# Kernel tuning notes

Measured on AMD Instinct MI355X. Metric: run time of the kernel, lower is better.

## Reference

```python
import jax, jax.numpy as jnp
import numpy as np

B, W, H = 128, 512, 512


def setup_inputs() -> dict:
    key = jax.random.key(0)
    ks = jax.random.split(key, 10)
    s = 1.0 / np.sqrt(H)
    return {
        "g": jax.random.normal(ks[0], (B, H), jnp.float32),
        "c_g": jax.random.normal(ks[1], (B, H), jnp.float32),
        "h": jax.random.normal(ks[2], (B, W, H), jnp.float32),
        "c": jax.random.normal(ks[3], (B, W, H), jnp.float32),
        "W_w": jax.random.normal(ks[4], (2 * H, H), jnp.float32) * s,
        "w_w": jax.random.normal(ks[5], (H, H), jnp.float32) * s,
        "U_w": jax.random.normal(ks[6], (2 * H, H), jnp.float32) * s,
        "U_b": jax.random.normal(ks[7], (2 * H,), jnp.float32) * s,
        "u_w": jax.random.normal(ks[8], (H, H), jnp.float32) * s,
        "u_b": jax.random.normal(ks[9], (H,), jnp.float32) * s,
    }


def reference(g, c_g, h, c, W_w, w_w, U_w, U_b, u_w, u_b):
    hid = w_w.shape[0]
    # attn_pooling: mean over word dim -> [B, H]
    h_avg = jnp.mean(h, axis=-2)
    # gates f, o: [B, H] each
    fo = jax.nn.sigmoid(g @ W_w.T + h_avg @ U_w.T + U_b)
    f, o = fo[..., :hid], fo[..., hid:]
    # per-word forget weights, softmax over word dim: [B, W, H]
    f_w = jax.nn.sigmoid((g @ w_w.T)[..., None, :] + h @ u_w.T + u_b)
    f_w = jax.nn.softmax(f_w, axis=-2)
    new_c = f * c_g + jnp.sum(c * f_w, axis=-2)
    new_g = o * jnp.tanh(new_c)
    return new_g, new_c
```

## Files before the change

kernel.cpp:

```cpp
#include <hip/hip_runtime.h>
#include <stdint.h>

#define BB 128
#define WW 512
#define HH 512
#define TILE 128
#define BK 64

typedef __attribute__((ext_vector_type(8))) short bf16x8;
typedef __attribute__((ext_vector_type(4))) float f32x4;

__device__ __forceinline__ float bf2f(unsigned short u) {
  union { unsigned int i; float f; } v;
  v.i = ((unsigned int)u) << 16;
  return v.f;
}
__device__ __forceinline__ unsigned int pack_bf2(float lo, float hi) {
  union { float f; unsigned int u; } a, b;
  a.f = lo; b.f = hi;
  return (a.u >> 16) | (b.u & 0xFFFF0000u);
}
__device__ __forceinline__ float dot4v(float4 u, float4 v) {
  return u.x * v.x + u.y * v.y + u.z * v.z + u.w * v.w;
}
__device__ __forceinline__ void gload_lds16(const void* src, void* lds_dst) {
  __builtin_amdgcn_global_load_lds(
      (const __attribute__((address_space(1))) unsigned int*)src,
      (__attribute__((address_space(3))) unsigned int*)lds_dst, 16, 0, 0);
}

__global__ __launch_bounds__(256) void k01(
    const float* __restrict__ g, const float* __restrict__ W_w,
    const float* __restrict__ w_w, const float* __restrict__ u_w,
    float* __restrict__ gw, float* __restrict__ gfo,
    unsigned short* __restrict__ u_wb) {
  __shared__ __align__(16) unsigned short As[TILE * BK];
  __shared__ __align__(16) unsigned short Bs[TILE * BK];
  const int bid = blockIdx.x;
  const int t = threadIdx.x;

  if (bid >= 12) {
    const int cid0 = (bid - 12) * 256 + t;
    for (int idx = cid0; idx < 32768; idx += 16384) {
      const int tile = idx >> 11;
      const int rem  = idx & 2047;
      const int row  = rem >> 3;
      const int eg   = (rem & 7) * 8;
      const int nh   = tile >> 3;
      const int kt   = tile & 7;
      const int c0   = kt * 64 + (eg ^ ((row & 7) << 3));
      const float4* sp = (const float4*)(u_w + (size_t)(nh * 256 + row) * HH + c0);
      float4 s0 = sp[0], s1 = sp[1];
      uint4 pv;
      pv.x = pack_bf2(s0.x, s0.y); pv.y = pack_bf2(s0.z, s0.w);
      pv.z = pack_bf2(s1.x, s1.y); pv.w = pack_bf2(s1.z, s1.w);
      *(uint4*)(u_wb + (size_t)idx * 8) = pv;
    }
    return;
  }

  const int nc = bid;
  const int lane = t & 63, wave = t >> 6;
  const int wm = wave >> 1, wn = wave & 1;
  const int l15 = lane & 15, quad = lane >> 4;

  const float* wsrc = (nc < 4) ? (w_w + (size_t)nc * TILE * HH)
                               : (W_w + (size_t)(nc - 4) * TILE * HH);

  const f32x4 zero = {0.f, 0.f, 0.f, 0.f};
  f32x4 acc[4][4];
#pragma unroll
  for (int i = 0; i < 4; ++i)
#pragma unroll
    for (int j = 0; j < 4; ++j) acc[i][j] = zero;

  const int srow = t >> 3;
  const int scol = (t & 7) * 8;

  for (int kt = 0; kt < 8; ++kt) {
    const int k0 = kt * BK;
#pragma unroll
    for (int p = 0; p < 4; ++p) {
      const int row = p * 32 + srow;
      const float4* ap = (const float4*)(g    + (size_t)row * HH + k0 + scol);
      const float4* bp = (const float4*)(wsrc + (size_t)row * HH + k0 + scol);
      float4 a0 = ap[0], a1 = ap[1], b0 = bp[0], b1 = bp[1];
      uint4 av, bv;
      av.x = pack_bf2(a0.x, a0.y); av.y = pack_bf2(a0.z, a0.w);
      av.z = pack_bf2(a1.x, a1.y); av.w = pack_bf2(a1.z, a1.w);
      bv.x = pack_bf2(b0.x, b0.y); bv.y = pack_bf2(b0.z, b0.w);
      bv.z = pack_bf2(b1.x, b1.y); bv.w = pack_bf2(b1.z, b1.w);
      *(uint4*)(As + row * BK + scol) = av;
      *(uint4*)(Bs + row * BK + scol) = bv;
    }
    __syncthreads();
#pragma unroll
    for (int ks = 0; ks < 2; ++ks) {
      bf16x8 af[4], bg[4];
#pragma unroll
      for (int i = 0; i < 4; ++i)
        af[i] = *(const bf16x8*)(As + (wm * 64 + i * 16 + l15) * BK + ks * 32 + quad * 8);
#pragma unroll
      for (int j = 0; j < 4; ++j)
        bg[j] = *(const bf16x8*)(Bs + (wn * 64 + j * 16 + l15) * BK + ks * 32 + quad * 8);
#pragma unroll
      for (int i = 0; i < 4; ++i)
#pragma unroll
        for (int j = 0; j < 4; ++j)
          acc[i][j] = __builtin_amdgcn_mfma_f32_16x16x32_bf16(af[i], bg[j], acc[i][j], 0, 0, 0);
    }
    __syncthreads();
  }

#pragma unroll
  for (int j = 0; j < 4; ++j) {
    const int nl = wn * 64 + j * 16 + l15;
#pragma unroll
    for (int i = 0; i < 4; ++i) {
#pragma unroll
      for (int r = 0; r < 4; ++r) {
        const int b = wm * 64 + i * 16 + quad * 4 + r;
        const float v = acc[i][j][r];
        if (nc < 4) gw[(size_t)b * HH + nc * TILE + nl] = v;
        else        gfo[(size_t)b * 2 * HH + (nc - 4) * TILE + nl] = v;
      }
    }
  }
}

__global__ __launch_bounds__(512, 4) void k2_fused(
    const float* __restrict__ h, const float* __restrict__ c,
    const unsigned short* __restrict__ u_wb, const float* __restrict__ u_b,
    const float* __restrict__ gw,
    float* __restrict__ hsumP, float* __restrict__ denP, float* __restrict__ numP) {
  __shared__ __align__(16) unsigned short Bs[256 * 64];
  __shared__ __align__(16) unsigned short As[128 * 64];
  __shared__ float colred[8][64];
  __shared__ float redD[2][256];
  __shared__ float redN[2][256];

  const int bid = blockIdx.x;
  const int b  = bid >> 3;
  const int wc = (bid >> 1) & 3;
  const int nh = bid & 1;
  const int t = threadIdx.x;
  const int lane = t & 63, wave = t >> 6;
  const int wm = wave >> 2, wn = wave & 3;
  const int l15 = lane & 15, quad = lane >> 4;

  const size_t hbase = ((size_t)b * WW + (size_t)wc * 128) * HH;
  const unsigned short* ubase = u_wb + (size_t)nh * 8 * 16384;

  const f32x4 zero = {0.f, 0.f, 0.f, 0.f};
  f32x4 acc[4][4];
#pragma unroll
  for (int i = 0; i < 4; ++i)
#pragma unroll
    for (int j = 0; j < 4; ++j) acc[i][j] = zero;

  const int srow = t >> 3;
  const int scol = (t & 7) * 8;

  for (int kt = 0; kt < 8; ++kt) {
    const int k0 = kt * 64;

    if (nh == 0 && kt > 0 && t < 64) {
      float tot = 0.f;
#pragma unroll
      for (int gq = 0; gq < 8; ++gq) tot += colred[gq][t];
      hsumP[((size_t)b * 4 + wc) * HH + (kt - 1) * 64 + t] = tot;
    }

#pragma unroll
    for (int it = 0; it < 4; ++it) {
      const int s = wave * 4 + it;
      const unsigned short* src =
          ubase + ((size_t)kt * 16384 + (size_t)s * 512 + (size_t)lane * 8);
      gload_lds16(src, Bs + (size_t)s * 512);
    }

#pragma unroll
    for (int p = 0; p < 2; ++p) {
      const int row = p * 64 + srow;
      const float4* ap = (const float4*)(h + hbase + (size_t)row * HH + k0 + scol);
      float4 a0 = ap[0], a1 = ap[1];
      uint4 av;
      av.x = pack_bf2(a0.x, a0.y); av.y = pack_bf2(a0.z, a0.w);
      av.z = pack_bf2(a1.x, a1.y); av.w = pack_bf2(a1.z, a1.w);
      *(uint4*)(As + row * 64 + (scol ^ ((row & 7) << 3))) = av;
    }
    __syncthreads();

    if (nh == 0) {
      const int col = t & 63, gq = t >> 6;
      float s = 0.f;
#pragma unroll
      for (int rr = 0; rr < 16; ++rr) {
        const int row = gq * 16 + rr;
        s += bf2f(As[row * 64 + (col ^ ((row & 7) << 3))]);
      }
      colred[gq][col] = s;
    }

#pragma unroll
    for (int ks = 0; ks < 2; ++ks) {
      bf16x8 af[4], bg[4];
#pragma unroll
      for (int i = 0; i < 4; ++i) {
        const int row = wm * 64 + i * 16 + l15;
        af[i] = *(const bf16x8*)(As + row * 64 + ((ks * 32 + quad * 8) ^ ((row & 7) << 3)));
      }
#pragma unroll
      for (int j = 0; j < 4; ++j) {
        const int row = wn * 64 + j * 16 + l15;
        bg[j] = *(const bf16x8*)(Bs + row * 64 + ((ks * 32 + quad * 8) ^ ((row & 7) << 3)));
      }
#pragma unroll
      for (int i = 0; i < 4; ++i)
#pragma unroll
        for (int j = 0; j < 4; ++j)
          acc[i][j] = __builtin_amdgcn_mfma_f32_16x16x32_bf16(af[i], bg[j], acc[i][j], 0, 0, 0);
    }
    __syncthreads();
  }

  if (nh == 0 && t < 64) {
    float tot = 0.f;
#pragma unroll
    for (int gq = 0; gq < 8; ++gq) tot += colred[gq][t];
    hsumP[((size_t)b * 4 + wc) * HH + 7 * 64 + t] = tot;
  }

  const int N0 = nh * 256;
#pragma unroll
  for (int j = 0; j < 4; ++j) {
    const int n = wn * 64 + j * 16 + l15;
    const float gwub = gw[(size_t)b * HH + N0 + n] + u_b[N0 + n];
    float dsum = 0.f, nsum = 0.f;
#pragma unroll
    for (int i = 0; i < 4; ++i) {
#pragma unroll
      for (int r = 0; r < 4; ++r) {
        const int m = wm * 64 + i * 16 + quad * 4 + r;
        const float z = acc[i][j][r] + gwub;
        const float sig = 1.f / (1.f + __expf(-z));
        const float e = __expf(sig);
        dsum += e;
        nsum += e * c[hbase + (size_t)m * HH + N0 + n];
      }
    }
    dsum += __shfl_xor(dsum, 16);
    dsum += __shfl_xor(dsum, 32);
    nsum += __shfl_xor(nsum, 16);
    nsum += __shfl_xor(nsum, 32);
    if (quad == 0) { redD[wm][n] = dsum; redN[wm][n] = nsum; }
  }
  __syncthreads();
  if (t < 256) {
    const size_t o = ((size_t)b * 4 + wc) * HH + N0 + t;
    denP[o] = redD[0][t] + redD[1][t];
    numP[o] = redN[0][t] + redN[1][t];
  }
}

__global__ __launch_bounds__(256) void k3_final(
    const float* __restrict__ c_g, const float* __restrict__ U_w,
    const float* __restrict__ U_b,
    const float* __restrict__ gfo, const float* __restrict__ hsumP,
    const float* __restrict__ denP, const float* __restrict__ numP,
    float* __restrict__ out) {
  __shared__ float logitL[256];
  __shared__ float ncL[128];
  __shared__ float oL[128];
  const int bid = blockIdx.x;
  const int b = bid >> 2, q = bid & 3;
  const int t = threadIdx.x;
  const int lane = t & 63, wave = t >> 6;

  float4 ha0 = {0.f, 0.f, 0.f, 0.f}, ha1 = {0.f, 0.f, 0.f, 0.f};
  {
    const float4* hp = (const float4*)(hsumP + (size_t)b * 4 * HH);
#pragma unroll
    for (int p = 0; p < 4; ++p) {
      float4 a = hp[p * 128 + lane * 2];
      float4 bq = hp[p * 128 + lane * 2 + 1];
      ha0.x += a.x; ha0.y += a.y; ha0.z += a.z; ha0.w += a.w;
      ha1.x += bq.x; ha1.y += bq.y; ha1.z += bq.z; ha1.w += bq.w;
    }
    const float sc = 1.f / (float)WW;
    ha0.x *= sc; ha0.y *= sc; ha0.z *= sc; ha0.w *= sc;
    ha1.x *= sc; ha1.y *= sc; ha1.z *= sc; ha1.w *= sc;
  }

#pragma unroll 2
  for (int r = 0; r < 64; ++r) {
    const int idx = wave * 64 + r;
    const int urow = (idx < 128) ? (q * 128 + idx) : (HH + q * 128 + (idx - 128));
    const float4* up = (const float4*)(U_w + (size_t)urow * HH);
    float4 u0 = up[lane * 2], u1 = up[lane * 2 + 1];
    float s = dot4v(u0, ha0) + dot4v(u1, ha1);
    s += __shfl_xor(s, 1);
    s += __shfl_xor(s, 2);
    s += __shfl_xor(s, 4);
    s += __shfl_xor(s, 8);
    s += __shfl_xor(s, 16);
    s += __shfl_xor(s, 32);
    if (lane == 0) logitL[idx] = s;
  }
  __syncthreads();

  const int isF = (t < 128);
  const int n = q * 128 + (t & 127);
  const int row = isF ? n : (HH + n);
  const float logit = logitL[t] + gfo[(size_t)b * 2 * HH + row] + U_b[row];
  const float sg = 1.f / (1.f + __expf(-logit));

  if (isF) {
    const float* dp = denP + (size_t)b * 4 * HH + n;
    const float* np = numP + (size_t)b * 4 * HH + n;
    const float den = dp[0] + dp[HH] + dp[2 * HH] + dp[3 * HH];
    const float num = np[0] + np[HH] + np[2 * HH] + np[3 * HH];
    const float ncv = sg * c_g[(size_t)b * HH + n] + num / den;
    ncL[t] = ncv;
    out[(size_t)BB * HH + (size_t)b * HH + n] = ncv;
  } else {
    oL[t - 128] = sg;
  }
  __syncthreads();
  if (isF) {
    out[(size_t)b * HH + n] = oL[t] * tanhf(ncL[t]);
  }
}

extern "C" void kernel_launch(void* const* d_in, const int* in_sizes, int n_in,
                              void* d_out, int out_size, void* d_ws, size_t ws_size,
                              hipStream_t stream) {
  const float* g   = (const float*)d_in[0];
  const float* c_g = (const float*)d_in[1];
  const float* h   = (const float*)d_in[2];
  const float* c   = (const float*)d_in[3];
  const float* W_w = (const float*)d_in[4];
  const float* w_w = (const float*)d_in[5];
  const float* U_w = (const float*)d_in[6];
  const float* U_b = (const float*)d_in[7];
  const float* u_w = (const float*)d_in[8];
  const float* u_b = (const float*)d_in[9];

  float* ws    = (float*)d_ws;
  float* gw    = ws;
  float* gfo   = gw + BB * HH;
  float* hsumP = gfo + (size_t)BB * 2 * HH;
  float* denP  = hsumP + (size_t)BB * 4 * HH;
  float* numP  = denP + (size_t)BB * 4 * HH;
  unsigned short* u_wb = (unsigned short*)(numP + (size_t)BB * 4 * HH);
  float* out = (float*)d_out;

  hipLaunchKernelGGL(k01, dim3(76), dim3(256), 0, stream, g, W_w, w_w, u_w, gw, gfo, u_wb);
  hipLaunchKernelGGL(k2_fused, dim3(1024), dim3(512), 0, stream,
                     h, c, u_wb, u_b, gw, hsumP, denP, numP);
  hipLaunchKernelGGL(k3_final, dim3(512), dim3(256), 0, stream,
                     c_g, U_w, U_b, gfo, hsumP, denP, numP, out);
}
```

Measured before the change: 383.0 us.

## Pre-convert h to swizzled bf16 once and stream it into LDS asynchronously

The first kernel gains extra blocks that convert each 128-row tile of h from fp32 to swizzled bf16 once. They write it to workspace and compute the per-chunk column sums of h there. The main kernel then fills LDS with direct global-to-LDS loads of both operands instead of loading and converting fp32 h in every block. This removes the duplicated conversion and hsum work in both column-half blocks. The cost is an extra 64 MB write and read of the bf16 copy. A fallback path, used when the workspace is too small, sums h with a slow serial loop.

```diff
diff --git a/kernel.cpp b/kernel.cpp
--- a/kernel.cpp
+++ b/kernel.cpp
@@ -29,15 +29,79 @@
       (__attribute__((address_space(3))) unsigned int*)lds_dst, 16, 0, 0);
 }
 
-__global__ __launch_bounds__(256) void k01(
+__global__ __launch_bounds__(256) void k0(
     const float* __restrict__ g, const float* __restrict__ W_w,
     const float* __restrict__ w_w, const float* __restrict__ u_w,
+    const float* __restrict__ h,
     float* __restrict__ gw, float* __restrict__ gfo,
-    unsigned short* __restrict__ u_wb) {
+    unsigned short* __restrict__ u_wb, unsigned short* __restrict__ hb,
+    float* __restrict__ hsumP, int primary) {
   __shared__ __align__(16) unsigned short As[TILE * BK];
   __shared__ __align__(16) unsigned short Bs[TILE * BK];
+  __shared__ float colred[4][64];
   const int bid = blockIdx.x;
   const int t = threadIdx.x;
+
+  if (bid >= 76) {
+    if (primary) {
+      const int id = bid - 76;
+      const float* hsrc = h + (size_t)id * TILE * HH;
+      unsigned short* hdst = hb + (size_t)id * (8 * 8192);
+      const int row = t >> 1;
+      const int cpart = (t & 1) * 32;
+      const int sw = (row & 7) << 3;
+      for (int kt = 0; kt < 8; ++kt) {
+        const float4* sp = (const float4*)(hsrc + (size_t)row * HH + kt * 64 + cpart);
+        float4 v[8];
+#pragma unroll
+        for (int q = 0; q < 8; ++q) v[q] = sp[q];
+#pragma unroll
+        for (int eg = 0; eg < 4; ++eg) {
+          uint4 pv;
+          pv.x = pack_bf2(v[2 * eg].x, v[2 * eg].y);
+          pv.y = pack_bf2(v[2 * eg].z, v[2 * eg].w);
+          pv.z = pack_bf2(v[2 * eg + 1].x, v[2 * eg + 1].y);
+          pv.w = pack_bf2(v[2 * eg + 1].z, v[2 * eg + 1].w);
+          const int off = row * 64 + ((cpart + eg * 8) ^ sw);
+          *(uint4*)(As + off) = pv;
+          *(uint4*)(hdst + (size_t)kt * 8192 + off) = pv;
+        }
+        __syncthreads();
+        {
+          const int col = t & 63, gq = t >> 6;
+          float s = 0.f;
+#pragma unroll
+          for (int rr = 0; rr < 32; ++rr) {
+            const int rw = gq * 32 + rr;
+            s += bf2f(As[rw * 64 + (col ^ ((rw & 7) << 3))]);
+          }
+          colred[gq][col] = s;
+        }
+        __syncthreads();
+        if (t < 64)
+          hsumP[(size_t)id * HH + kt * 64 + t] =
+              colred[0][t] + colred[1][t] + colred[2][t] + colred[3][t];
+        __syncthreads();
+      }
+    } else {
+      const int b = bid - 76;
+      const float* hp = h + (size_t)b * WW * HH;
+      const int col0 = t * 2;
+      float s0 = 0.f, s1 = 0.f;
+      for (int w = 0; w < WW; ++w) {
+        const float2 v = *(const float2*)(hp + (size_t)w * HH + col0);
+        s0 += v.x; s1 += v.y;
+      }
+      hsumP[(size_t)b * 4 * HH + col0] = s0;
+      hsumP[(size_t)b * 4 * HH + col0 + 1] = s1;
+#pragma unroll
+      for (int p = 1; p < 4; ++p) {
+        hsumP[((size_t)b * 4 + p) * HH + col0] = 0.f;
+        hsumP[((size_t)b * 4 + p) * HH + col0 + 1] = 0.f;
+      }
+    }
+    return;
+  }
 
   if (bid >= 12) {
     const int cid0 = (bid - 12) * 256 + t;
@@ -78,12 +142,12 @@
   const int scol = (t & 7) * 8;
 
   for (int kt = 0; kt < 8; ++kt) {
-    const int k0 = kt * BK;
+    const int k0i = kt * BK;
 #pragma unroll
     for (int p = 0; p < 4; ++p) {
       const int row = p * 32 + srow;
-      const float4* ap = (const float4*)(g    + (size_t)row * HH + k0 + scol);
-      const float4* bp = (const float4*)(wsrc + (size_t)row * HH + k0 + scol);
+      const float4* ap = (const float4*)(g    + (size_t)row * HH + k0i + scol);
+      const float4* bp = (const float4*)(wsrc + (size_t)row * HH + k0i + scol);
       float4 a0 = ap[0], a1 = ap[1], b0 = bp[0], b1 = bp[1];
       uint4 av, bv;
       av.x = pack_bf2(a0.x, a0.y); av.y = pack_bf2(a0.z, a0.w);
@@ -128,16 +192,15 @@
   }
 }
 
-__global__ __launch_bounds__(512, 4) void k2_fused(
-    const float* __restrict__ h, const float* __restrict__ c,
+__global__ __launch_bounds__(512, 4) void k2p(
+    const unsigned short* __restrict__ hb, const float* __restrict__ c,
     const unsigned short* __restrict__ u_wb, const float* __restrict__ u_b,
     const float* __restrict__ gw,
-    float* __restrict__ hsumP, float* __restrict__ denP, float* __restrict__ numP) {
+    float* __restrict__ denP, float* __restrict__ numP) {
   __shared__ __align__(16) unsigned short Bs[256 * 64];
   __shared__ __align__(16) unsigned short As[128 * 64];
-  __shared__ float colred[8][64];
-  __shared__ float redD[2][256];
-  __shared__ float redN[2][256];
+  float (*redD)[256] = (float (*)[256])(void*)As;
+  float (*redN)[256] = (float (*)[256])(void*)(As + 1024);
 
   const int bid = blockIdx.x;
   const int b  = bid >> 3;
@@ -149,6 +212,7 @@
   const int l15 = lane & 15, quad = lane >> 4;
 
   const size_t hbase = ((size_t)b * WW + (size_t)wc * 128) * HH;
+  const unsigned short* hbA = hb + (size_t)(bid >> 1) * (8 * 8192);
   const unsigned short* ubase = u_wb + (size_t)nh * 8 * 16384;
 
   const f32x4 zero = {0.f, 0.f, 0.f, 0.f};
@@ -158,31 +222,119 @@
 #pragma unroll
     for (int j = 0; j < 4; ++j) acc[i][j] = zero;
 
+  for (int kt = 0; kt < 8; ++kt) {
+#pragma unroll
+    for (int it = 0; it < 2; ++it) {
+      const int s = wave * 2 + it;
+      gload_lds16(hbA + (size_t)kt * 8192 + (size_t)s * 512 + (size_t)lane * 8,
+                  As + (size_t)s * 512);
+    }
+#pragma unroll
+    for (int it = 0; it < 4; ++it) {
+      const int s = wave * 4 + it;
+      gload_lds16(ubase + (size_t)kt * 16384 + (size_t)s * 512 + (size_t)lane * 8,
+                  Bs + (size_t)s * 512);
+    }
+    __syncthreads();
+
+#pragma unroll
+    for (int ks = 0; ks < 2; ++ks) {
+      bf16x8 af[4], bg[4];
+#pragma unroll
+      for (int i = 0; i < 4; ++i) {
+        const int row = wm * 64 + i * 16 + l15;
+        af[i] = *(const bf16x8*)(As + row * 64 + ((ks * 32 + quad * 8) ^ ((row & 7) << 3)));
+      }
+#pragma unroll
+      for (int j = 0; j < 4; ++j) {
+        const int row = wn * 64 + j * 16 + l15;
+        bg[j] = *(const bf16x8*)(Bs + row * 64 + ((ks * 32 + quad * 8) ^ ((row & 7) << 3)));
+      }
+#pragma unroll
+      for (int i = 0; i < 4; ++i)
+#pragma unroll
+        for (int j = 0; j < 4; ++j)
+          acc[i][j] = __builtin_amdgcn_mfma_f32_16x16x32_bf16(af[i], bg[j], acc[i][j], 0, 0, 0);
+    }
+    __syncthreads();
+  }
+
+  const int N0 = nh * 256;
+#pragma unroll
+  for (int j = 0; j < 4; ++j) {
+    const int n = wn * 64 + j * 16 + l15;
+    const float gwub = gw[(size_t)b * HH + N0 + n] + u_b[N0 + n];
+    float dsum = 0.f, nsum = 0.f;
+#pragma unroll
+    for (int i = 0; i < 4; ++i) {
+#pragma unroll
+      for (int r = 0; r < 4; ++r) {
+        const int m = wm * 64 + i * 16 + quad * 4 + r;
+        const float z = acc[i][j][r] + gwub;
+        const float sig = 1.f / (1.f + __expf(-z));
+        const float e = __expf(sig);
+        dsum += e;
+        nsum += e * c[hbase + (size_t)m * HH + N0 + n];
+      }
+    }
+    dsum += __shfl_xor(dsum, 16);
+    dsum += __shfl_xor(dsum, 32);
+    nsum += __shfl_xor(nsum, 16);
+    nsum += __shfl_xor(nsum, 32);
+    if (quad == 0) { redD[wm][n] = dsum; redN[wm][n] = nsum; }
+  }
+  __syncthreads();
+  if (t < 256) {
+    const size_t o = ((size_t)b * 4 + wc) * HH + N0 + t;
+    denP[o] = redD[0][t] + redD[1][t];
+    numP[o] = redN[0][t] + redN[1][t];
+  }
+}
+
+__global__ __launch_bounds__(512, 4) void k2f(
+    const float* __restrict__ h, const float* __restrict__ c,
+    const unsigned short* __restrict__ u_wb, const float* __restrict__ u_b,
+    const float* __restrict__ gw,
+    float* __restrict__ denP, float* __restrict__ numP) {
+  __shared__ __align__(16) unsigned short Bs[256 * 64];
+  __shared__ __align__(16) unsigned short As[128 * 64];
+  float (*redD)[256] = (float (*)[256])(void*)As;
+  float (*redN)[256] = (float (*)[256])(void*)(As + 1024);
+
+  const int bid = blockIdx.x;
+  const int b  = bid >> 3;
+  const int wc = (bid >> 1) & 3;
+  const int nh = bid & 1;
+  const int t = threadIdx.x;
+  const int lane = t & 63, wave = t >> 6;
+  const int wm = wave >> 2, wn = wave & 3;
+  const int l15 = lane & 15, quad = lane >> 4;
+
+  const size_t hbase = ((size_t)b * WW + (size_t)wc * 128) * HH;
+  const unsigned short* ubase = u_wb + (size_t)nh * 8 * 16384;
+
+  const f32x4 zero = {0.f, 0.f, 0.f, 0.f};
+  f32x4 acc[4][4];
+#pragma unroll
+  for (int i = 0; i < 4; ++i)
+#pragma unroll
+    for (int j = 0; j < 4; ++j) acc[i][j] = zero;
+
   const int srow = t >> 3;
   const int scol = (t & 7) * 8;
 
   for (int kt = 0; kt < 8; ++kt) {
-    const int k0 = kt * 64;
-
-    if (nh == 0 && kt > 0 && t < 64) {
-      float tot = 0.f;
-#pragma unroll
-      for (int gq = 0; gq < 8; ++gq) tot += colred[gq][t];
-      hsumP[((size_t)b * 4 + wc) * HH + (kt - 1) * 64 + t] = tot;
-    }
-
+    const int k0i = kt * 64;
 #pragma unroll
     for (int it = 0; it < 4; ++it) {
       const int s = wave * 4 + it;
-      const unsigned short* src =
-          ubase + ((size_t)kt * 16384 + (size_t)s * 512 + (size_t)lane * 8);
-      gload_lds16(src, Bs + (size_t)s * 512);
-    }
-
+      gload_lds16(ubase + ((size_t)kt * 16384 + (size_t)s * 512 + (size_t)lane * 8),
+                  Bs + (size_t)s * 512);
+    }
 #pragma unroll
     for (int p = 0; p < 2; ++p) {
       const int row = p * 64 + srow;
-      const float4* ap = (const float4*)(h + hbase + (size_t)row * HH + k0 + scol);
+      const float4* ap = (const float4*)(h + hbase + (size_t)row * HH + k0i + scol);
       float4 a0 = ap[0], a1 = ap[1];
       uint4 av;
       av.x = pack_bf2(a0.x, a0.y); av.y = pack_bf2(a0.z, a0.w);
@@ -190,18 +342,6 @@
       *(uint4*)(As + row * 64 + (scol ^ ((row & 7) << 3))) = av;
     }
     __syncthreads();
-
-    if (nh == 0) {
-      const int col = t & 63, gq = t >> 6;
-      float s = 0.f;
-#pragma unroll
-      for (int rr = 0; rr < 16; ++rr) {
-        const int row = gq * 16 + rr;
-        s += bf2f(As[row * 64 + (col ^ ((row & 7) << 3))]);
-      }
-      colred[gq][col] = s;
-    }
-
 #pragma unroll
     for (int ks = 0; ks < 2; ++ks) {
       bf16x8 af[4], bg[4];
@@ -222,13 +362,6 @@
           acc[i][j] = __builtin_amdgcn_mfma_f32_16x16x32_bf16(af[i], bg[j], acc[i][j], 0, 0, 0);
     }
     __syncthreads();
-  }
-
-  if (nh == 0 && t < 64) {
-    float tot = 0.f;
-#pragma unroll
-    for (int gq = 0; gq < 8; ++gq) tot += colred[gq][t];
-    hsumP[((size_t)b * 4 + wc) * HH + 7 * 64 + t] = tot;
   }
 
   const int N0 = nh * 256;
@@ -353,11 +486,21 @@
   float* denP  = hsumP + (size_t)BB * 4 * HH;
   float* numP  = denP + (size_t)BB * 4 * HH;
   unsigned short* u_wb = (unsigned short*)(numP + (size_t)BB * 4 * HH);
+  unsigned short* hb = u_wb + 262144;
   float* out = (float*)d_out;
 
-  hipLaunchKernelGGL(k01, dim3(76), dim3(256), 0, stream, g, W_w, w_w, u_w, gw, gfo, u_wb);
-  hipLaunchKernelGGL(k2_fused, dim3(1024), dim3(512), 0, stream,
-                     h, c, u_wb, u_b, gw, hsumP, denP, numP);
+  const size_t need = ((size_t)((float*)hb - ws)) * 4 + (size_t)BB * WW * HH * 2;
+  const int primary = (ws_size >= need) ? 1 : 0;
+
+  hipLaunchKernelGGL(k0, dim3(primary ? 588 : 204), dim3(256), 0, stream,
+                     g, W_w, w_w, u_w, h, gw, gfo, u_wb, hb, hsumP, primary);
+  if (primary) {
+    hipLaunchKernelGGL(k2p, dim3(1024), dim3(512), 0, stream,
+                       hb, c, u_wb, u_b, gw, denP, numP);
+  } else {
+    hipLaunchKernelGGL(k2f, dim3(1024), dim3(512), 0, stream,
+                       h, c, u_wb, u_b, gw, denP, numP);
+  }
   hipLaunchKernelGGL(k3_final, dim3(512), dim3(256), 0, stream,
                      c_g, U_w, U_b, gfo, hsumP, denP, numP, out);
 }
```

Measured after the change: 395.3 us. 3.2% more time.
